# Kernel optimization log

Hardware: AMD Instinct MI355X
Metric: run time of the kernel (lower is better)

## Reference

```python
import jax, jax.numpy as jnp
from jax import lax
import numpy as np
import math

N_BLOCK = 10
CH = 64          # channels (nf)
IN_CH = 3        # input image channels
K = 3            # kernel size
COND_CH = 128    # conv_index='22' condition channel
B, H, W = 4, 128, 128


def setup_inputs() -> dict:
    key = jax.random.key(0)
    ks = jax.random.split(key, 8)
    x = jax.random.normal(ks[0], (B, IN_CH, H, W), jnp.float32)
    condition_feature = jax.random.normal(ks[1], (B, COND_CH, 1, 1), jnp.float32)
    # BaseConv2d params are torch.randn (initialize_weights skips BaseConv2d/EqualLinear)
    in_w = jax.random.normal(ks[2], (CH, IN_CH, K, K), jnp.float32)
    in_b = jnp.zeros((CH,), jnp.float32)
    blk_w = jax.random.normal(ks[3], (N_BLOCK, 2, CH, CH, K, K), jnp.float32)
    blk_b = jnp.zeros((N_BLOCK, 2, CH), jnp.float32)
    mod_w = jax.random.normal(ks[4], (N_BLOCK * 2, CH, COND_CH), jnp.float32)  # EqualLinear weights
    mod_b = jnp.ones((N_BLOCK * 2, CH), jnp.float32)                           # bias_init=1
    up_w = jax.random.normal(ks[5], (2, 4 * CH, CH, K, K), jnp.float32)        # two x2 pixel-shuffle stages
    up_b = jnp.zeros((2, 4 * CH), jnp.float32)
    out_w = jax.random.normal(ks[6], (IN_CH, CH, K, K), jnp.float32)
    out_b = jnp.zeros((IN_CH,), jnp.float32)
    return dict(x=x, condition_feature=condition_feature, in_w=in_w, in_b=in_b,
                blk_w=blk_w, blk_b=blk_b, mod_w=mod_w, mod_b=mod_b,
                up_w=up_w, up_b=up_b, out_w=out_w, out_b=out_b)


def _conv(x, w, b):
    out = lax.conv_general_dilated(x, w, (1, 1), [(K // 2, K // 2)] * 2,
                                   dimension_numbers=('NCHW', 'OIHW', 'NCHW'))
    return out + b[None, :, None, None]


def _mod_conv(x, w, bias, cond, scale):
    # x [b,c,h,w]; w [out,in,k,k]; cond [b,1,in,1,1] -> per-sample modulated weights
    wmod = w[None] * scale * cond  # [b,out,in,k,k]
    conv1 = lambda xi, wi: lax.conv_general_dilated(
        xi[None], wi, (1, 1), [(K // 2, K // 2)] * 2,
        dimension_numbers=('NCHW', 'OIHW', 'NCHW'))[0]
    out = jax.vmap(conv1)(x, wmod)  # groups=batch grouped conv
    # faithful to torch.repeat_interleave(bias, repeats=b) split across groups
    b_ = x.shape[0]
    bmat = jnp.repeat(bias, b_).reshape(b_, bias.shape[0])
    return out + bmat[:, :, None, None]


def _pixel_shuffle(x, r):
    b, c, h, w = x.shape
    C = c // (r * r)
    return x.reshape(b, C, r, r, h, w).transpose(0, 1, 4, 2, 5, 3).reshape(b, C, h * r, w * r)


def reference(x, condition_feature, in_w, in_b, blk_w, blk_b, mod_w, mod_b,
              up_w, up_b, out_w, out_b):
    b = x.shape[0]
    s_in = 1.0 / math.sqrt(IN_CH * K * K)
    s64 = 1.0 / math.sqrt(CH * K * K)
    s_lin = 1.0 / math.sqrt(COND_CH)

    # Modulations: 20 EqualLinears on [b,128] -> [10,2,b,1,64,1,1]
    cf = condition_feature.reshape(b, COND_CH)
    feats = jnp.einsum('bc,moc->mbo', cf, mod_w) * s_lin + mod_b[:, None, :]
    cond_feats = feats.reshape(N_BLOCK, 2, b, 1, CH, 1, 1)

    fea = _conv(x, in_w * s_in, in_b)
    for i in range(N_BLOCK):
        res = _mod_conv(fea, blk_w[i, 0], blk_b[i, 0], cond_feats[i, 0], s64)
        res = jax.nn.relu(res)
        res = _mod_conv(res, blk_w[i, 1], blk_b[i, 1], cond_feats[i, 1], s64)
        fea = res + fea  # residual_lr = 1
    for j in range(2):  # scale=4 -> two (conv, PixelShuffle(2)) stages
        fea = _conv(fea, up_w[j] * s64, up_b[j])
        fea = _pixel_shuffle(fea, 2)
    out = _conv(fea, out_w * s64, out_b)
    return out
```

## Files before the change

kernel.cpp:

```cpp
#include <hip/hip_runtime.h>
#include <math.h>

typedef unsigned short u16;
typedef unsigned int u32;
typedef float f32x4 __attribute__((ext_vector_type(4)));
typedef _Float16 f16;
typedef f16 f16x8 __attribute__((ext_vector_type(8)));
typedef f16 f16x4 __attribute__((ext_vector_type(4)));
typedef u32 u32x4 __attribute__((ext_vector_type(4)));


__device__ u16  g_bufT[(size_t)4*128*128*64];
__device__ float g_bufR[(size_t)4*128*128*64];
__device__ u16  g_bufB[(size_t)4*128*128*64];
__device__ u16  g_bufC[(size_t)4*4*256*256*16];
__device__ u16  g_bufE[(size_t)4*4*512*512*16];
__device__ float g_mod[20*4*64];
__device__ f16 g_wblk[(size_t)20*4*36864];
__device__ f16 g_wup[(size_t)2*4*36864];
__device__ f16 g_wout[9216];
__device__ u16 g_zero[8];

__device__ __forceinline__ void gll16(const void* g, void* l) {
    __builtin_amdgcn_global_load_lds(
        (const __attribute__((address_space(1))) unsigned*)g,
        (__attribute__((address_space(3))) unsigned*)l, 16, 0, 0);
}

__global__ void mod_kernel(const float* __restrict__ cf,
                           const float* __restrict__ mw,
                           const float* __restrict__ mb,
                           float* __restrict__ mod) {
    int m = blockIdx.x, b = blockIdx.y, o = threadIdx.x;
    const float* wrow = mw + (m * 64 + o) * 128;
    const float* cfb  = cf + b * 128;
    float s = 0.f;
#pragma unroll 8
    for (int c = 0; c < 128; ++c) s = fmaf(cfb[c], wrow[c], s);
    mod[(m * 4 + b) * 64 + o] = s * 0.08838834764831845f + mb[m * 64 + o];
}

__global__ void prep_blk_kernel(const float* __restrict__ bw,
                                const float* __restrict__ mod,
                                f16* __restrict__ wp) {
    int c = blockIdx.x, b = blockIdx.y;
    const float s64 = 1.0f / 24.0f;
    size_t base = (size_t)(c * 4 + b) * 36864;
    for (int idx = threadIdx.x; idx < 36864; idx += 256) {
        int j = idx & 7, l = (idx >> 3) & 63;
        int frag = idx >> 9;
        int mt = frag & 3, kfr = frag >> 2;
        int kf = kfr & 1, tap = kfr >> 1;
        int oc = mt * 16 + (l & 15);
        int ic = kf * 32 + (l >> 4) * 8 + j;
        float val = bw[((size_t)(c * 64 + oc) * 64 + ic) * 9 + tap] * s64 *
                    mod[(c * 4 + b) * 64 + ic];
        wp[base + idx] = (f16)val;
    }
}

__global__ void prep_up_kernel(const float* __restrict__ uw, f16* __restrict__ wp) {
    int st = blockIdx.x, ocg = blockIdx.y;
    const float s64 = 1.0f / 24.0f;
    size_t base = (size_t)(st * 4 + ocg) * 36864;
    for (int idx = threadIdx.x; idx < 36864; idx += 256) {
        int j = idx & 7, l = (idx >> 3) & 63;
        int frag = idx >> 9;
        int mt = frag & 3, kfr = frag >> 2;
        int kf = kfr & 1, tap = kfr >> 1;
        int oc = ocg * 64 + mt * 16 + (l & 15);
        int ic = kf * 32 + (l >> 4) * 8 + j;
        wp[base + idx] = (f16)(uw[((size_t)(st * 256 + oc) * 64 + ic) * 9 + tap] * s64);
    }
}

__global__ void prep_out_kernel(const float* __restrict__ ow, f16* __restrict__ wp) {
    const float s64 = 1.0f / 24.0f;
    for (int idx = threadIdx.x; idx < 9216; idx += 256) {
        int j = idx & 7, l = (idx >> 3) & 63;
        int frag = idx >> 9;
        int kf = frag & 1, tap = frag >> 1;
        int oc = l & 15;
        int ic = kf * 32 + (l >> 4) * 8 + j;
        float val = (oc < 3) ? ow[((size_t)(oc * 64) + ic) * 9 + tap] * s64 : 0.f;
        wp[idx] = (f16)val;
    }
}

__global__ __launch_bounds__(256) void in_conv_kernel(
    const float* __restrict__ in, const float* __restrict__ wgt,
    const float* __restrict__ bias, float* __restrict__ outR,
    u16* __restrict__ outT) {
    __shared__ float slds[3][34][35];
    __shared__ float wlds[3 * 9 * 16];
    const int H = 128, W = 128;
    const int tid = threadIdx.x, x = tid & 31, yb = tid >> 5;
    const int b = blockIdx.z >> 2, ocb = (blockIdx.z & 3) * 16;
    const int tY = blockIdx.y * 32, tX = blockIdx.x * 32;
    const float s_in = 0.19245008972987526f;

    float acc[16][4];
#pragma unroll
    for (int oc = 0; oc < 16; ++oc)
#pragma unroll
        for (int k = 0; k < 4; ++k) acc[oc][k] = 0.f;

    for (int idx = tid; idx < 3 * 34 * 34; idx += 256) {
        int ic = idx / (34 * 34), p = idx % (34 * 34);
        int r = p / 34, c = p % 34;
        int gy = tY + r - 1, gx = tX + c - 1;
        float v = 0.f;
        if (gy >= 0 && gy < H && gx >= 0 && gx < W)
            v = in[((b * 3 + ic) * H + gy) * W + gx] * s_in;
        slds[ic][r][c] = v;
    }
    for (int idx = tid; idx < 3 * 9 * 16; idx += 256) {
        int oc = idx & 15, tap = (idx >> 4) % 9, ic = idx / 144;
        wlds[idx] = wgt[((ocb + oc) * 3 + ic) * 9 + tap];
    }
    __syncthreads();

#pragma unroll
    for (int ic = 0; ic < 3; ++ic)
#pragma unroll
        for (int dy = 0; dy < 3; ++dy)
#pragma unroll
            for (int dx = 0; dx < 3; ++dx) {
                float xv[4];
#pragma unroll
                for (int k = 0; k < 4; ++k)
                    xv[k] = slds[ic][yb + 8 * k + dy][x + dx];
                const float* wrow = &wlds[(ic * 9 + dy * 3 + dx) * 16];
#pragma unroll
                for (int oc = 0; oc < 16; ++oc) {
                    float wv = wrow[oc];
#pragma unroll
                    for (int k = 0; k < 4; ++k) acc[oc][k] = fmaf(wv, xv[k], acc[oc][k]);
                }
            }

#pragma unroll
    for (int oc = 0; oc < 16; ++oc) {
        int goc = ocb + oc;
        float bv = bias[goc];
#pragma unroll
        for (int k = 0; k < 4; ++k) {
            int gy = tY + yb + 8 * k, gx = tX + x;
            size_t pixG = ((size_t)b * H + gy) * W + gx;
            float v = acc[oc][k] + bv;
            outR[pixG * 64 + goc] = v;
            outT[pixG * 64 + goc] = __builtin_bit_cast(u16, (f16)v);
        }
    }
}

template <int CG, int RG, int MG, int MT, int ROWS, int INMODE, int OUTMODE, int LB>
__global__ __launch_bounds__(CG* RG* MG * 64, LB) void mconv(
    const u16* __restrict__ inh, const f16* __restrict__ wp,
    const float* __restrict__ bias, float* __restrict__ rbuf,
    void* __restrict__ outv, u16* __restrict__ outT,
    int H, int W, int OCG, int wp_bstride, size_t in_pl, size_t out_pl)
{
    constexpr int TC = CG * 16, TR = RG * ROWS;
    constexpr int CST = TC + 2, RST = TR + 2;
    constexpr int PXT = RST * CST;
    constexpr int MT_W = MT / MG;
    constexpr int NW = CG * RG * MG;
    constexpr int NTHR = NW * 64;
    constexpr int SB_H = 8 * PXT * 8;
    constexpr int NP = 2 * TR * TC;
    constexpr int SMEM_H = (OUTMODE == 2 && 16 * NP * 2 > SB_H) ? 16 * NP * 2 : SB_H;

    __shared__ __align__(16) u16 smem[SMEM_H];

    const int tid = threadIdx.x;
    const int lane = tid & 63, wv = tid >> 6;
    const int lcol = lane & 15, lk8 = lane >> 4;
    const int cg = (CG > 1) ? (wv % CG) : 0;
    const int rg = (wv / CG) % RG;
    const int mg = wv / (CG * RG);
    const int b = blockIdx.z / OCG, ocg = blockIdx.z % OCG;
    const int y0 = blockIdx.y * TR, x0 = blockIdx.x * TC;
    const f16* wpb = wp + (size_t)b * wp_bstride + (size_t)ocg * 36864;

    auto loadA = [&](int s, f16x8(&A)[3][MT_W]) {
        int kf = s / 3, dx = s - kf * 3;
#pragma unroll
        for (int dy = 0; dy < 3; ++dy)
#pragma unroll
            for (int m = 0; m < MT_W; ++m) {
                int frag = ((dy * 3 + dx) * 2 + kf) * MT + mg * MT_W + m;
                A[dy][m] = *(const f16x8*)(wpb + (size_t)frag * 512 + (size_t)lane * 8);
            }
    };

    f16x8 Ab[2][3][MT_W];
    loadA(0, Ab[0]);

    for (int g = tid; g < 8 * PXT; g += NTHR) {
        int pl = g / PXT, px = g - pl * PXT;
        int t = px / CST, c = px - t * CST;
        int gy = y0 + t - 1, gx = x0 + c - 1;
        const void* src = g_zero;
        if (gy >= 0 && gy < H && gx >= 0 && gx < W) {
            size_t pix = ((size_t)b * H + gy) * W + gx;
            int ic = pl * 8;
            if (INMODE == 1)
                src = inh + pix * 64 + ic;
            else
                src = inh + (size_t)(ic >> 4) * in_pl + pix * 16 + (ic & 15);
        }
        gll16(src, smem + (size_t)g * 8);
    }
    __syncthreads();

    f32x4 acc[ROWS][MT_W];
#pragma unroll
    for (int r = 0; r < ROWS; ++r)
#pragma unroll
        for (int m = 0; m < MT_W; ++m) acc[r][m] = (f32x4)0.f;

#pragma unroll
    for (int s = 0; s < 6; ++s) {
        if (s < 5) loadA(s + 1, Ab[(s + 1) & 1]);
        const int kf = s / 3, dx = s - kf * 3;
        const u16* bp = smem + (size_t)(kf * 4 + lk8) * PXT * 8;
        const int pcol = cg * 16 + dx + lcol;
#pragma unroll
        for (int iy = 0; iy < ROWS + 2; ++iy) {
            int px = (rg * ROWS + iy) * CST + pcol;
            f16x8 Bf = *(const f16x8*)(bp + (size_t)px * 8);
#pragma unroll
            for (int dy = 0; dy < 3; ++dy) {
                int r = iy - dy;
                if (r >= 0 && r < ROWS) {
#pragma unroll
                    for (int m = 0; m < MT_W; ++m)
                        acc[r][m] = __builtin_amdgcn_mfma_f32_16x16x32_f16(
                            Ab[s & 1][dy][m], Bf, acc[r][m], 0, 0, 0);
                }
            }
        }
    }

    if (OUTMODE == 0 || OUTMODE == 1) {
        u16* outh = (u16*)outv;
#pragma unroll
        for (int r = 0; r < ROWS; ++r) {
            int gy = y0 + rg * ROWS + r, gx = x0 + cg * 16 + lcol;
            size_t pixG = ((size_t)b * H + gy) * W + gx;
#pragma unroll
            for (int m = 0; m < MT_W; ++m) {
                int oc0 = (mg * MT_W + m) * 16 + lk8 * 4;
                f32x4 v = acc[r][m] + *(const f32x4*)(bias + oc0);
                if (OUTMODE == 0) {
                    f16x4 o;
#pragma unroll
                    for (int j = 0; j < 4; ++j) o[j] = (f16)fmaxf(v[j], 0.f);
                    *(f16x4*)(outh + pixG * 64 + oc0) = o;
                } else {
                    float* rp = rbuf + pixG * 64 + oc0;
                    f32x4 rv = *(const f32x4*)rp;
                    v += rv;
                    *(f32x4*)rp = v;
                    f16x4 o;
#pragma unroll
                    for (int j = 0; j < 4; ++j) o[j] = (f16)v[j];
                    *(f16x4*)(outT + pixG * 64 + oc0) = o;
                }
            }
        }
    } else if (OUTMODE == 2) {
        __syncthreads();
        u32* sT = (u32*)smem;
#pragma unroll
        for (int r = 0; r < ROWS; ++r) {
#pragma unroll
            for (int m = 0; m < MT_W; ++m) {
                int oc0 = (mg * MT_W + m) * 16 + lk8 * 4;
                int cc = (mg * MT_W + m) * 4 + lk8;
                f32x4 v = acc[r][m] + *(const f32x4*)(bias + ocg * 64 + oc0);
                int oy = 2 * (rg * ROWS + r);
#pragma unroll
                for (int jp = 0; jp < 2; ++jp) {
                    f16 e0 = (f16)v[jp * 2], e1 = (f16)v[jp * 2 + 1];
                    u32 w = (u32)__builtin_bit_cast(u16, e0) |
                            ((u32)__builtin_bit_cast(u16, e1) << 16);
                    sT[cc * NP + (oy + jp) * TC + cg * 16 + lcol] = w;
                }
            }
        }
        __syncthreads();
        u16* outh = (u16*)outv + (size_t)ocg * out_pl;
        const int H2 = 2 * H, W2 = 2 * W;
#pragma unroll
        for (int it = 0; it < NP / NTHR; ++it) {
            int p = tid + it * NTHR;
            int oy = p / TC, xp = p - oy * TC;
            u32 tv[16];
#pragma unroll
            for (int c = 0; c < 16; ++c) tv[c] = sT[c * NP + p];
            u32 q0[8], q1[8];
#pragma unroll
            for (int c2 = 0; c2 < 8; ++c2) {
                q0[c2] = (tv[2 * c2] & 0xffffu) | (tv[2 * c2 + 1] << 16);
                q1[c2] = (tv[2 * c2] >> 16) | (tv[2 * c2 + 1] & 0xffff0000u);
            }
            int gy2 = 2 * y0 + oy, gx2 = 2 * x0 + 2 * xp;
            u16* dst = outh + (((size_t)b * H2 + gy2) * W2 + gx2) * 16;
            *(u32x4*)(dst)      = *(u32x4*)(q0);
            *(u32x4*)(dst + 8)  = *(u32x4*)(q0 + 4);
            *(u32x4*)(dst + 16) = *(u32x4*)(q1);
            *(u32x4*)(dst + 24) = *(u32x4*)(q1 + 4);
        }
    } else {
        float* outp = (float*)outv;
        if (lk8 == 0) {
#pragma unroll
            for (int r = 0; r < ROWS; ++r) {
                int gy = y0 + rg * ROWS + r, gx = x0 + cg * 16 + lcol;
#pragma unroll
                for (int j = 0; j < 3; ++j) {
                    float v = acc[r][0][j] + bias[j];
                    outp[(((size_t)b * 3 + j) * H + gy) * W + gx] = v;
                }
            }
        }
    }
}

extern "C" void kernel_launch(void* const* d_in, const int* in_sizes, int n_in,
                              void* d_out, int out_size, void* d_ws, size_t ws_size,
                              hipStream_t stream) {
    const float* x     = (const float*)d_in[0];
    const float* cf    = (const float*)d_in[1];
    const float* in_w  = (const float*)d_in[2];
    const float* in_b  = (const float*)d_in[3];
    const float* blk_w = (const float*)d_in[4];
    const float* blk_b = (const float*)d_in[5];
    const float* mod_w = (const float*)d_in[6];
    const float* mod_b = (const float*)d_in[7];
    const float* up_w  = (const float*)d_in[8];
    const float* up_b  = (const float*)d_in[9];
    const float* out_w = (const float*)d_in[10];
    const float* out_b = (const float*)d_in[11];
    float* outp = (float*)d_out;

    u16 *bufT, *bufB, *bufC, *bufE;
    float *bufR, *modp;
    f16 *wblk, *wup, *wout;
    hipGetSymbolAddress((void**)&bufT, HIP_SYMBOL(g_bufT));
    hipGetSymbolAddress((void**)&bufR, HIP_SYMBOL(g_bufR));
    hipGetSymbolAddress((void**)&bufB, HIP_SYMBOL(g_bufB));
    hipGetSymbolAddress((void**)&bufC, HIP_SYMBOL(g_bufC));
    hipGetSymbolAddress((void**)&bufE, HIP_SYMBOL(g_bufE));
    hipGetSymbolAddress((void**)&modp, HIP_SYMBOL(g_mod));
    hipGetSymbolAddress((void**)&wblk, HIP_SYMBOL(g_wblk));
    hipGetSymbolAddress((void**)&wup,  HIP_SYMBOL(g_wup));
    hipGetSymbolAddress((void**)&wout, HIP_SYMBOL(g_wout));

    mod_kernel<<<dim3(20, 4), 64, 0, stream>>>(cf, mod_w, mod_b, modp);
    prep_blk_kernel<<<dim3(20, 4), 256, 0, stream>>>(blk_w, modp, wblk);
    prep_up_kernel<<<dim3(2, 4), 256, 0, stream>>>(up_w, wup);
    prep_out_kernel<<<1, 256, 0, stream>>>(out_w, wout);

    in_conv_kernel<<<dim3(4, 4, 16), 256, 0, stream>>>(x, in_w, in_b, bufR, bufT);

    const size_t PLC = (size_t)4 * 256 * 256 * 16;
    const size_t PLE = (size_t)4 * 512 * 512 * 16;

    for (int i = 0; i < 10; ++i) {
        mconv<1, 2, 2, 4, 4, 1, 0, 3><<<dim3(8, 16, 4), 256, 0, stream>>>(
            bufT, wblk + (size_t)(2 * i) * 4 * 36864, blk_b + (2 * i) * 64,
            nullptr, bufB, nullptr, 128, 128, 1, 36864, 0, 0);
        mconv<1, 2, 2, 4, 4, 1, 1, 3><<<dim3(8, 16, 4), 256, 0, stream>>>(
            bufB, wblk + (size_t)(2 * i + 1) * 4 * 36864, blk_b + (2 * i + 1) * 64,
            bufR, nullptr, bufT, 128, 128, 1, 36864, 0, 0);
    }

    mconv<2, 1, 2, 4, 8, 1, 2, 3><<<dim3(4, 16, 16), 256, 0, stream>>>(
        bufT, wup, up_b, nullptr, bufC, nullptr, 128, 128, 4, 0, 0, PLC);
    mconv<2, 1, 2, 4, 8, 2, 2, 3><<<dim3(8, 32, 16), 256, 0, stream>>>(
        bufC, wup + (size_t)4 * 36864, up_b + 256, nullptr, bufE, nullptr,
        256, 256, 4, 0, PLC, PLE);
    mconv<2, 2, 1, 1, 4, 2, 3, 4><<<dim3(16, 64, 4), 256, 0, stream>>>(
        bufE, wout, out_b, nullptr, outp, nullptr, 512, 512, 1, 0, PLE, 0);
}
```

Before: 543.7 us.

## Loop output-channel groups inside conv blocks and switch activations to planar layout

The upsampling convs now loop over all four 64-channel output groups inside one block, so each input tile is staged into LDS once instead of four times. Weights for the next group are prefetched across the group boundary. All intermediate fp16 activations move from pixel-major 64-channel layout to a 16-channel planar layout, and the LDS plane stride is padded, presumably to reduce bank conflicts. The pixel-shuffle epilogue now writes through a smaller staging buffer in row chunks, which adds extra barriers, and launch bounds and tile shapes for the up and out convs change.

```diff
diff --git a/kernel.cpp b/kernel.cpp
--- a/kernel.cpp
+++ b/kernel.cpp
@@ -94,6 +94,7 @@
     __shared__ float slds[3][34][35];
     __shared__ float wlds[3 * 9 * 16];
     const int H = 128, W = 128;
+    const size_t PLT = (size_t)4 * 128 * 128 * 16;
     const int tid = threadIdx.x, x = tid & 31, yb = tid >> 5;
     const int b = blockIdx.z >> 2, ocb = (blockIdx.z & 3) * 16;
     const int tY = blockIdx.y * 32, tX = blockIdx.x * 32;
@@ -149,29 +150,32 @@
             size_t pixG = ((size_t)b * H + gy) * W + gx;
             float v = acc[oc][k] + bv;
             outR[pixG * 64 + goc] = v;
-            outT[pixG * 64 + goc] = __builtin_bit_cast(u16, (f16)v);
+            outT[(size_t)(goc >> 4) * PLT + pixG * 16 + (goc & 15)] =
+                __builtin_bit_cast(u16, (f16)v);
         }
     }
 }
 
-template <int CG, int RG, int MG, int MT, int ROWS, int INMODE, int OUTMODE, int LB>
+template <int CG, int RG, int MG, int MT, int ROWS, int NOCG, int OUTMODE, int LB>
 __global__ __launch_bounds__(CG* RG* MG * 64, LB) void mconv(
     const u16* __restrict__ inh, const f16* __restrict__ wp,
     const float* __restrict__ bias, float* __restrict__ rbuf,
     void* __restrict__ outv, u16* __restrict__ outT,
-    int H, int W, int OCG, int wp_bstride, size_t in_pl, size_t out_pl)
+    int H, int W, int wp_bstride, size_t in_pl, size_t out_pl)
 {
     constexpr int TC = CG * 16, TR = RG * ROWS;
     constexpr int CST = TC + 2, RST = TR + 2;
     constexpr int PXT = RST * CST;
+    constexpr int PXS = PXT + ((2 - (PXT & 7) + 8) & 7);
     constexpr int MT_W = MT / MG;
     constexpr int NW = CG * RG * MG;
     constexpr int NTHR = NW * 64;
-    constexpr int SB_H = 8 * PXT * 8;
-    constexpr int NP = 2 * TR * TC;
-    constexpr int SMEM_H = (OUTMODE == 2 && 16 * NP * 2 > SB_H) ? 16 * NP * 2 : SB_H;
-
-    __shared__ __align__(16) u16 smem[SMEM_H];
+    constexpr int SB_H = 8 * PXS * 8;
+    constexpr int NPP = 8 * TC + 8;
+    constexpr int ST_H = (OUTMODE == 2) ? 16 * NPP * 2 : 0;
+
+    __shared__ __align__(16) u16 smem[SB_H + ST_H];
+    u32* sT = (u32*)(smem + SB_H);
 
     const int tid = threadIdx.x;
     const int lane = tid & 63, wv = tid >> 6;
@@ -179,150 +183,153 @@
     const int cg = (CG > 1) ? (wv % CG) : 0;
     const int rg = (wv / CG) % RG;
     const int mg = wv / (CG * RG);
-    const int b = blockIdx.z / OCG, ocg = blockIdx.z % OCG;
+    const int b = blockIdx.z;
     const int y0 = blockIdx.y * TR, x0 = blockIdx.x * TC;
-    const f16* wpb = wp + (size_t)b * wp_bstride + (size_t)ocg * 36864;
-
-    auto loadA = [&](int s, f16x8(&A)[3][MT_W]) {
+
+    auto loadA = [&](int ocg, int s, f16x8(&A)[3][MT_W]) {
         int kf = s / 3, dx = s - kf * 3;
+        const f16* base = wp + (size_t)b * wp_bstride + (size_t)ocg * 36864;
 #pragma unroll
         for (int dy = 0; dy < 3; ++dy)
 #pragma unroll
             for (int m = 0; m < MT_W; ++m) {
                 int frag = ((dy * 3 + dx) * 2 + kf) * MT + mg * MT_W + m;
-                A[dy][m] = *(const f16x8*)(wpb + (size_t)frag * 512 + (size_t)lane * 8);
+                A[dy][m] = *(const f16x8*)(base + (size_t)frag * 512 + (size_t)lane * 8);
             }
     };
 
     f16x8 Ab[2][3][MT_W];
-    loadA(0, Ab[0]);
-
-    for (int g = tid; g < 8 * PXT; g += NTHR) {
-        int pl = g / PXT, px = g - pl * PXT;
+    loadA(0, 0, Ab[0]);
+
+    for (int g = tid; g < 8 * PXS; g += NTHR) {
+        int pl = g / PXS, px = g - pl * PXS;
         int t = px / CST, c = px - t * CST;
         int gy = y0 + t - 1, gx = x0 + c - 1;
         const void* src = g_zero;
-        if (gy >= 0 && gy < H && gx >= 0 && gx < W) {
+        if (px < PXT && gy >= 0 && gy < H && gx >= 0 && gx < W) {
             size_t pix = ((size_t)b * H + gy) * W + gx;
-            int ic = pl * 8;
-            if (INMODE == 1)
-                src = inh + pix * 64 + ic;
-            else
-                src = inh + (size_t)(ic >> 4) * in_pl + pix * 16 + (ic & 15);
+            src = inh + (size_t)(pl >> 1) * in_pl + pix * 16 + (pl & 1) * 8;
         }
         gll16(src, smem + (size_t)g * 8);
     }
     __syncthreads();
 
-    f32x4 acc[ROWS][MT_W];
-#pragma unroll
-    for (int r = 0; r < ROWS; ++r)
-#pragma unroll
-        for (int m = 0; m < MT_W; ++m) acc[r][m] = (f32x4)0.f;
-
-#pragma unroll
-    for (int s = 0; s < 6; ++s) {
-        if (s < 5) loadA(s + 1, Ab[(s + 1) & 1]);
-        const int kf = s / 3, dx = s - kf * 3;
-        const u16* bp = smem + (size_t)(kf * 4 + lk8) * PXT * 8;
-        const int pcol = cg * 16 + dx + lcol;
-#pragma unroll
-        for (int iy = 0; iy < ROWS + 2; ++iy) {
-            int px = (rg * ROWS + iy) * CST + pcol;
-            f16x8 Bf = *(const f16x8*)(bp + (size_t)px * 8);
-#pragma unroll
-            for (int dy = 0; dy < 3; ++dy) {
-                int r = iy - dy;
-                if (r >= 0 && r < ROWS) {
-#pragma unroll
-                    for (int m = 0; m < MT_W; ++m)
-                        acc[r][m] = __builtin_amdgcn_mfma_f32_16x16x32_f16(
-                            Ab[s & 1][dy][m], Bf, acc[r][m], 0, 0, 0);
+#pragma unroll 1
+    for (int o = 0; o < NOCG; ++o) {
+        f32x4 acc[ROWS][MT_W];
+#pragma unroll
+        for (int r = 0; r < ROWS; ++r)
+#pragma unroll
+            for (int m = 0; m < MT_W; ++m) acc[r][m] = (f32x4)0.f;
+
+#pragma unroll
+        for (int s = 0; s < 6; ++s) {
+            if (s < 5) loadA(o, s + 1, Ab[(s + 1) & 1]);
+            else if (o + 1 < NOCG) loadA(o + 1, 0, Ab[0]);
+            const int kf = s / 3, dx = s - kf * 3;
+            const u16* bp = smem + (size_t)(kf * 4 + lk8) * PXS * 8;
+            const int pcol = cg * 16 + dx + lcol;
+#pragma unroll
+            for (int iy = 0; iy < ROWS + 2; ++iy) {
+                int px = (rg * ROWS + iy) * CST + pcol;
+                f16x8 Bf = *(const f16x8*)(bp + (size_t)px * 8);
+#pragma unroll
+                for (int dy = 0; dy < 3; ++dy) {
+                    int r = iy - dy;
+                    if (r >= 0 && r < ROWS) {
+#pragma unroll
+                        for (int m = 0; m < MT_W; ++m)
+                            acc[r][m] = __builtin_amdgcn_mfma_f32_16x16x32_f16(
+                                Ab[s & 1][dy][m], Bf, acc[r][m], 0, 0, 0);
+                    }
                 }
             }
         }
-    }
-
-    if (OUTMODE == 0 || OUTMODE == 1) {
-        u16* outh = (u16*)outv;
-#pragma unroll
-        for (int r = 0; r < ROWS; ++r) {
-            int gy = y0 + rg * ROWS + r, gx = x0 + cg * 16 + lcol;
-            size_t pixG = ((size_t)b * H + gy) * W + gx;
-#pragma unroll
-            for (int m = 0; m < MT_W; ++m) {
-                int oc0 = (mg * MT_W + m) * 16 + lk8 * 4;
-                f32x4 v = acc[r][m] + *(const f32x4*)(bias + oc0);
-                if (OUTMODE == 0) {
-                    f16x4 o;
-#pragma unroll
-                    for (int j = 0; j < 4; ++j) o[j] = (f16)fmaxf(v[j], 0.f);
-                    *(f16x4*)(outh + pixG * 64 + oc0) = o;
-                } else {
-                    float* rp = rbuf + pixG * 64 + oc0;
-                    f32x4 rv = *(const f32x4*)rp;
-                    v += rv;
-                    *(f32x4*)rp = v;
-                    f16x4 o;
-#pragma unroll
-                    for (int j = 0; j < 4; ++j) o[j] = (f16)v[j];
-                    *(f16x4*)(outT + pixG * 64 + oc0) = o;
-                }
-            }
-        }
-    } else if (OUTMODE == 2) {
-        __syncthreads();
-        u32* sT = (u32*)smem;
-#pragma unroll
-        for (int r = 0; r < ROWS; ++r) {
-#pragma unroll
-            for (int m = 0; m < MT_W; ++m) {
-                int oc0 = (mg * MT_W + m) * 16 + lk8 * 4;
-                int cc = (mg * MT_W + m) * 4 + lk8;
-                f32x4 v = acc[r][m] + *(const f32x4*)(bias + ocg * 64 + oc0);
-                int oy = 2 * (rg * ROWS + r);
-#pragma unroll
-                for (int jp = 0; jp < 2; ++jp) {
-                    f16 e0 = (f16)v[jp * 2], e1 = (f16)v[jp * 2 + 1];
-                    u32 w = (u32)__builtin_bit_cast(u16, e0) |
-                            ((u32)__builtin_bit_cast(u16, e1) << 16);
-                    sT[cc * NP + (oy + jp) * TC + cg * 16 + lcol] = w;
-                }
-            }
-        }
-        __syncthreads();
-        u16* outh = (u16*)outv + (size_t)ocg * out_pl;
-        const int H2 = 2 * H, W2 = 2 * W;
-#pragma unroll
-        for (int it = 0; it < NP / NTHR; ++it) {
-            int p = tid + it * NTHR;
-            int oy = p / TC, xp = p - oy * TC;
-            u32 tv[16];
-#pragma unroll
-            for (int c = 0; c < 16; ++c) tv[c] = sT[c * NP + p];
-            u32 q0[8], q1[8];
-#pragma unroll
-            for (int c2 = 0; c2 < 8; ++c2) {
-                q0[c2] = (tv[2 * c2] & 0xffffu) | (tv[2 * c2 + 1] << 16);
-                q1[c2] = (tv[2 * c2] >> 16) | (tv[2 * c2 + 1] & 0xffff0000u);
-            }
-            int gy2 = 2 * y0 + oy, gx2 = 2 * x0 + 2 * xp;
-            u16* dst = outh + (((size_t)b * H2 + gy2) * W2 + gx2) * 16;
-            *(u32x4*)(dst)      = *(u32x4*)(q0);
-            *(u32x4*)(dst + 8)  = *(u32x4*)(q0 + 4);
-            *(u32x4*)(dst + 16) = *(u32x4*)(q1);
-            *(u32x4*)(dst + 24) = *(u32x4*)(q1 + 4);
-        }
-    } else {
-        float* outp = (float*)outv;
-        if (lk8 == 0) {
+
+        if (OUTMODE == 0 || OUTMODE == 1) {
+            u16* outh = (u16*)outv;
 #pragma unroll
             for (int r = 0; r < ROWS; ++r) {
                 int gy = y0 + rg * ROWS + r, gx = x0 + cg * 16 + lcol;
-#pragma unroll
-                for (int j = 0; j < 3; ++j) {
-                    float v = acc[r][0][j] + bias[j];
-                    outp[(((size_t)b * 3 + j) * H + gy) * W + gx] = v;
+                size_t pixG = ((size_t)b * H + gy) * W + gx;
+#pragma unroll
+                for (int m = 0; m < MT_W; ++m) {
+                    int oc0 = (mg * MT_W + m) * 16 + lk8 * 4;
+                    f32x4 v = acc[r][m] + *(const f32x4*)(bias + oc0);
+                    if (OUTMODE == 0) {
+                        f16x4 ov;
+#pragma unroll
+                        for (int j = 0; j < 4; ++j) ov[j] = (f16)fmaxf(v[j], 0.f);
+                        *(f16x4*)(outh + (size_t)(oc0 >> 4) * out_pl + pixG * 16 + (oc0 & 15)) = ov;
+                    } else {
+                        float* rp = rbuf + pixG * 64 + oc0;
+                        f32x4 rv = *(const f32x4*)rp;
+                        v += rv;
+                        *(f32x4*)rp = v;
+                        f16x4 ov;
+#pragma unroll
+                        for (int j = 0; j < 4; ++j) ov[j] = (f16)v[j];
+                        *(f16x4*)(outT + (size_t)(oc0 >> 4) * out_pl + pixG * 16 + (oc0 & 15)) = ov;
+                    }
+                }
+            }
+        } else if (OUTMODE == 2) {
+            u16* outh = (u16*)outv + (size_t)o * out_pl;
+            const int H2 = 2 * H, W2 = 2 * W;
+#pragma unroll
+            for (int p = 0; p < TR / 4; ++p) {
+#pragma unroll
+                for (int r = 0; r < ROWS; ++r) {
+                    int ri = rg * ROWS + r;
+                    if (ri >= p * 4 && ri < p * 4 + 4) {
+#pragma unroll
+                        for (int m = 0; m < MT_W; ++m) {
+                            int oc0 = (mg * MT_W + m) * 16 + lk8 * 4;
+                            int cc = (mg * MT_W + m) * 4 + lk8;
+                            f32x4 v = acc[r][m] + *(const f32x4*)(bias + o * 64 + oc0);
+                            int oyl = 2 * (ri - p * 4);
+#pragma unroll
+                            for (int jp = 0; jp < 2; ++jp) {
+                                f16 e0 = (f16)v[jp * 2], e1 = (f16)v[jp * 2 + 1];
+                                u32 w = (u32)__builtin_bit_cast(u16, e0) |
+                                        ((u32)__builtin_bit_cast(u16, e1) << 16);
+                                sT[cc * NPP + (oyl + jp) * TC + cg * 16 + lcol] = w;
+                            }
+                        }
+                    }
+                }
+                __syncthreads();
+                if (tid < 8 * TC) {
+                    int oyl = tid / TC, xp = tid - oyl * TC;
+                    u32 tv[16];
+#pragma unroll
+                    for (int c = 0; c < 16; ++c) tv[c] = sT[c * NPP + oyl * TC + xp];
+                    u32 q0[8], q1[8];
+#pragma unroll
+                    for (int c2 = 0; c2 < 8; ++c2) {
+                        q0[c2] = (tv[2 * c2] & 0xffffu) | (tv[2 * c2 + 1] << 16);
+                        q1[c2] = (tv[2 * c2] >> 16) | (tv[2 * c2 + 1] & 0xffff0000u);
+                    }
+                    int gy2 = 2 * y0 + p * 8 + oyl, gx2 = 2 * x0 + 2 * xp;
+                    u16* dst = outh + (((size_t)b * H2 + gy2) * W2 + gx2) * 16;
+                    *(u32x4*)(dst)      = *(u32x4*)(q0);
+                    *(u32x4*)(dst + 8)  = *(u32x4*)(q0 + 4);
+                    *(u32x4*)(dst + 16) = *(u32x4*)(q1);
+                    *(u32x4*)(dst + 24) = *(u32x4*)(q1 + 4);
+                }
+                __syncthreads();
+            }
+        } else {
+            float* outp = (float*)outv;
+            if (lk8 == 0) {
+#pragma unroll
+                for (int r = 0; r < ROWS; ++r) {
+                    int gy = y0 + rg * ROWS + r, gx = x0 + cg * 16 + lcol;
+#pragma unroll
+                    for (int j = 0; j < 3; ++j) {
+                        float v = acc[r][0][j] + bias[j];
+                        outp[(((size_t)b * 3 + j) * H + gy) * W + gx] = v;
+                    }
                 }
             }
         }
@@ -366,23 +373,24 @@
 
     in_conv_kernel<<<dim3(4, 4, 16), 256, 0, stream>>>(x, in_w, in_b, bufR, bufT);
 
+    const size_t PLT = (size_t)4 * 128 * 128 * 16;
     const size_t PLC = (size_t)4 * 256 * 256 * 16;
     const size_t PLE = (size_t)4 * 512 * 512 * 16;
 
     for (int i = 0; i < 10; ++i) {
         mconv<1, 2, 2, 4, 4, 1, 0, 3><<<dim3(8, 16, 4), 256, 0, stream>>>(
             bufT, wblk + (size_t)(2 * i) * 4 * 36864, blk_b + (2 * i) * 64,
-            nullptr, bufB, nullptr, 128, 128, 1, 36864, 0, 0);
+            nullptr, bufB, nullptr, 128, 128, 36864, PLT, PLT);
         mconv<1, 2, 2, 4, 4, 1, 1, 3><<<dim3(8, 16, 4), 256, 0, stream>>>(
             bufB, wblk + (size_t)(2 * i + 1) * 4 * 36864, blk_b + (2 * i + 1) * 64,
-            bufR, nullptr, bufT, 128, 128, 1, 36864, 0, 0);
-    }
-
-    mconv<2, 1, 2, 4, 8, 1, 2, 3><<<dim3(4, 16, 16), 256, 0, stream>>>(
-        bufT, wup, up_b, nullptr, bufC, nullptr, 128, 128, 4, 0, 0, PLC);
-    mconv<2, 1, 2, 4, 8, 2, 2, 3><<<dim3(8, 32, 16), 256, 0, stream>>>(
+            bufR, nullptr, bufT, 128, 128, 36864, PLT, PLT);
+    }
+
+    mconv<1, 2, 2, 4, 4, 4, 2, 3><<<dim3(8, 16, 4), 256, 0, stream>>>(
+        bufT, wup, up_b, nullptr, bufC, nullptr, 128, 128, 0, PLT, PLC);
+    mconv<2, 1, 2, 4, 8, 4, 2, 2><<<dim3(8, 32, 4), 256, 0, stream>>>(
         bufC, wup + (size_t)4 * 36864, up_b + 256, nullptr, bufE, nullptr,
-        256, 256, 4, 0, PLC, PLE);
-    mconv<2, 2, 1, 1, 4, 2, 3, 4><<<dim3(16, 64, 4), 256, 0, stream>>>(
-        bufE, wout, out_b, nullptr, outp, nullptr, 512, 512, 1, 0, PLE, 0);
-}
+        256, 256, 0, PLC, PLE);
+    mconv<2, 2, 1, 1, 4, 1, 3, 3><<<dim3(16, 64, 4), 256, 0, stream>>>(
+        bufE, wout, out_b, nullptr, outp, nullptr, 512, 512, 0, PLE, 0);
+}
```

Result: faster. 486.8 us (-10.5%).
